# Optimization experiments

Hardware: AMD Instinct MI355X
Metric: run time of the kernel (lower is better)

## Reference

```python
import jax, jax.numpy as jnp
import numpy as np

EMBED = 1024
HIDDEN = 2048
BATCH = 8192


def setup_inputs() -> dict:
    key = jax.random.key(0)
    ks = jax.random.split(key, 14)
    D = EMBED + HIDDEN
    s = 1.0 / np.sqrt(D)
    s2 = 1.0 / np.sqrt(HIDDEN)
    return {
        "x": jax.random.normal(ks[0], (BATCH, EMBED), jnp.float32),
        "short_term": jax.random.normal(ks[1], (BATCH, HIDDEN), jnp.float32),
        "long_term": jax.random.normal(ks[2], (BATCH, HIDDEN), jnp.float32),
        "W_f": jax.random.normal(ks[3], (HIDDEN, D), jnp.float32) * s,
        "b_f": jax.random.normal(ks[4], (HIDDEN,), jnp.float32) * s,
        "W_i": jax.random.normal(ks[5], (HIDDEN, D), jnp.float32) * s,
        "b_i": jax.random.normal(ks[6], (HIDDEN,), jnp.float32) * s,
        "W_c": jax.random.normal(ks[7], (HIDDEN, D), jnp.float32) * s,
        "b_c": jax.random.normal(ks[8], (HIDDEN,), jnp.float32) * s,
        "W_o": jax.random.normal(ks[9], (HIDDEN, D), jnp.float32) * s,
        "b_o": jax.random.normal(ks[10], (HIDDEN,), jnp.float32) * s,
        "W_h2o": jax.random.normal(ks[11], (HIDDEN, HIDDEN), jnp.float32) * s2,
        "b_h2o": jax.random.normal(ks[12], (HIDDEN,), jnp.float32) * s2,
    }


def reference(x, short_term, long_term, W_f, b_f, W_i, b_i, W_c, b_c, W_o, b_o, W_h2o, b_h2o):
    combined = jnp.concatenate([x, short_term], axis=-1)  # [B, E+H]
    # Fuse the four gate linears into one GEMM: [B, E+H] @ [E+H, 4H]
    W_all = jnp.concatenate([W_f, W_i, W_c, W_o], axis=0)  # [4H, E+H]
    b_all = jnp.concatenate([b_f, b_i, b_c, b_o], axis=0)  # [4H]
    gates = combined @ W_all.T + b_all                     # [B, 4H]
    f, i, C, o = jnp.split(gates, 4, axis=-1)
    f = jax.nn.sigmoid(f)
    i = jax.nn.sigmoid(i)
    C = jnp.tanh(C)
    o = jax.nn.sigmoid(o)
    C_new = f * long_term + i * C                          # [B, H]
    C_out = jnp.tanh(C_new @ W_h2o.T + b_h2o)
    output = C_out * o
    return output, C_new
```

## Files before the change

### kernel.cpp

```cpp
#include <hip/hip_runtime.h>
#include <hip/hip_bf16.h>

typedef __bf16 bf16x8 __attribute__((ext_vector_type(8)));
typedef float f32x4 __attribute__((ext_vector_type(4)));

static constexpr int BATCH  = 8192;
static constexpr int EMBED  = 1024;
static constexpr int HIDDEN = 2048;
static constexpr int KD     = EMBED + HIDDEN;

__device__ __forceinline__ float sigm(float x) { return 1.0f / (1.0f + __expf(-x)); }
__device__ __forceinline__ float tanh_fast(float x) { return 2.0f / (1.0f + __expf(-2.0f * x)) - 1.0f; }

__device__ __forceinline__ bf16x8 loadcvt8(const float* __restrict__ p) {
  f32x4 lo = *(const f32x4*)p;
  f32x4 hi = *(const f32x4*)(p + 4);
  bf16x8 r;
  r[0] = (__bf16)lo[0]; r[1] = (__bf16)lo[1]; r[2] = (__bf16)lo[2]; r[3] = (__bf16)lo[3];
  r[4] = (__bf16)hi[0]; r[5] = (__bf16)hi[1]; r[6] = (__bf16)hi[2]; r[7] = (__bf16)hi[3];
  return r;
}

__device__ __forceinline__ void glds16(const void* g, void* l) {
  __builtin_amdgcn_global_load_lds((const __attribute__((address_space(1))) void*)g,
                                   (__attribute__((address_space(3))) void*)l, 16, 0, 0);
}

__global__ __launch_bounds__(256) void cvtA_kernel(const float* __restrict__ x,
                                                   const float* __restrict__ st,
                                                   __bf16* __restrict__ dst) {
  const long i8 = ((long)blockIdx.x * 256 + threadIdx.x) * 8;
  const int r = (int)(i8 / KD);
  const int c = (int)(i8 - (long)r * KD);
  const float* s = (c < EMBED) ? (x + (long)r * EMBED + c)
                               : (st + (long)r * HIDDEN + (c - EMBED));
  *(bf16x8*)(dst + i8) = loadcvt8(s);
}

__global__ __launch_bounds__(256) void cvtW_kernel(const float* __restrict__ Wf,
                                                   const float* __restrict__ Wi,
                                                   const float* __restrict__ Wc,
                                                   const float* __restrict__ Wo,
                                                   __bf16* __restrict__ dst) {
  const int g = blockIdx.y;
  const float* s = (g == 0) ? Wf : (g == 1) ? Wi : (g == 2) ? Wc : Wo;
  const long off = ((long)blockIdx.x * 256 + threadIdx.x) * 8;
  *(bf16x8*)(dst + (long)g * HIDDEN * KD + off) = loadcvt8(s + off);
}

__global__ __launch_bounds__(256) void cvtC_kernel(const float* __restrict__ s,
                                                   __bf16* __restrict__ d) {
  const long off = ((long)blockIdx.x * 256 + threadIdx.x) * 8;
  *(bf16x8*)(d + off) = loadcvt8(s + off);
}

__global__ __launch_bounds__(256, 3) void lstm_gates_kernel(
    const __bf16* __restrict__ A,
    const __bf16* __restrict__ W4,
    const float* __restrict__ lt,
    const float* __restrict__ bfp, const float* __restrict__ bip,
    const float* __restrict__ bcp, const float* __restrict__ bop,
    float* __restrict__ out1, float* __restrict__ out2,
    __bf16* __restrict__ flt, __bf16* __restrict__ ig)
{
  __shared__ __align__(16) __bf16 sA[128 * 32];
  __shared__ __align__(16) __bf16 sB[128 * 32];

  const int tid  = threadIdx.x;
  const int lane = tid & 63;
  const int wave = tid >> 6;
  const int waveM = wave >> 1;
  const int waveN = wave & 1;
  const int gate = blockIdx.z;

  const int row0 = blockIdx.y * 128;
  const int n0   = blockIdx.x * 128;

  const __bf16* __restrict__ Wg = W4 + (long)gate * HIDDEN * KD;

  const int sRow = lane >> 2;
  const int sCol = (lane & 3) * 8;
  const long aA0 = (long)(row0 + wave * 32 +      sRow) * KD + sCol;
  const long aA1 = (long)(row0 + wave * 32 + 16 + sRow) * KD + sCol;
  const long aB0 = (long)(n0   + wave * 32 +      sRow) * KD + sCol;
  const long aB1 = (long)(n0   + wave * 32 + 16 + sRow) * KD + sCol;
  __bf16* lA0 = sA + wave * 1024;
  __bf16* lA1 = sA + wave * 1024 + 512;
  __bf16* lB0 = sB + wave * 1024;
  __bf16* lB1 = sB + wave * 1024 + 512;

  const int kr = (lane >> 4) * 8;
  const int rA = (waveM * 64 + (lane & 15)) * 32 + kr;
  const int rB = (waveN * 64 + (lane & 15)) * 32 + kr;

  f32x4 acc[4][4];
#pragma unroll
  for (int fm = 0; fm < 4; ++fm)
#pragma unroll
    for (int fn = 0; fn < 4; ++fn)
      acc[fm][fn] = (f32x4){0.f, 0.f, 0.f, 0.f};

  for (int k0 = 0; k0 < KD; k0 += 32) {
    __syncthreads();
    glds16(A  + aA0 + k0, lA0);
    glds16(A  + aA1 + k0, lA1);
    glds16(Wg + aB0 + k0, lB0);
    glds16(Wg + aB1 + k0, lB1);
    __syncthreads();

    bf16x8 a[4], b[4];
#pragma unroll
    for (int f = 0; f < 4; ++f) {
      a[f] = *(const bf16x8*)(sA + rA + f * 16 * 32);
      b[f] = *(const bf16x8*)(sB + rB + f * 16 * 32);
    }
#pragma unroll
    for (int fm = 0; fm < 4; ++fm)
#pragma unroll
      for (int fn = 0; fn < 4; ++fn)
        acc[fm][fn] = __builtin_amdgcn_mfma_f32_16x16x32_bf16(a[fm], b[fn], acc[fm][fn], 0, 0, 0);
  }

  const int colB = n0 + waveN * 64 + (lane & 15);
  const int rowB = row0 + waveM * 64 + ((lane >> 4) << 2);

  const float* bias = (gate == 0) ? bfp : (gate == 1) ? bip : (gate == 2) ? bcp : bop;

#pragma unroll
  for (int fn = 0; fn < 4; ++fn) {
    const int col = colB + fn * 16;
    const float bv = bias[col];
#pragma unroll
    for (int fm = 0; fm < 4; ++fm) {
#pragma unroll
      for (int rr = 0; rr < 4; ++rr) {
        const int row = rowB + fm * 16 + rr;
        const size_t idx = (size_t)row * HIDDEN + col;
        const float v = acc[fm][fn][rr] + bv;
        if (gate == 0) {
          flt[idx] = (__bf16)(sigm(v) * lt[idx]);
        } else if (gate == 1) {
          ig[idx] = (__bf16)sigm(v);
        } else if (gate == 2) {
          out2[idx] = tanh_fast(v);
        } else {
          out1[idx] = sigm(v);
        }
      }
    }
  }
}

__global__ __launch_bounds__(256) void lstm_cell_kernel(
    const __bf16* __restrict__ flt, const __bf16* __restrict__ ig,
    float* __restrict__ out2 ,
    __bf16* __restrict__ cnb)
{
  const long i8 = ((long)blockIdx.x * 256 + threadIdx.x) * 8;
  bf16x8 f8 = *(const bf16x8*)(flt + i8);
  bf16x8 i8v = *(const bf16x8*)(ig + i8);
  f32x4 t0 = *(const f32x4*)(out2 + i8);
  f32x4 t1 = *(const f32x4*)(out2 + i8 + 4);
  f32x4 c0, c1;
  bf16x8 cb;
#pragma unroll
  for (int j = 0; j < 4; ++j) {
    c0[j] = (float)f8[j] + (float)i8v[j] * t0[j];
    c1[j] = (float)f8[j + 4] + (float)i8v[j + 4] * t1[j];
    cb[j] = (__bf16)c0[j];
    cb[j + 4] = (__bf16)c1[j];
  }
  *(f32x4*)(out2 + i8) = c0;
  *(f32x4*)(out2 + i8 + 4) = c1;
  *(bf16x8*)(cnb + i8) = cb;
}

__global__ __launch_bounds__(256, 3) void lstm_out_kernel(
    const __bf16* __restrict__ cnb, const __bf16* __restrict__ Whb,
    const float* __restrict__ bh, float* __restrict__ out1)
{
  __shared__ __align__(16) __bf16 sA[128 * 32];
  __shared__ __align__(16) __bf16 sB[128 * 32];

  const int tid  = threadIdx.x;
  const int lane = tid & 63;
  const int wave = tid >> 6;
  const int waveM = wave >> 1;
  const int waveN = wave & 1;

  const int row0 = blockIdx.y * 128;
  const int n0   = blockIdx.x * 128;

  const int sRow = lane >> 2;
  const int sCol = (lane & 3) * 8;
  const long aA0 = (long)(row0 + wave * 32 +      sRow) * HIDDEN + sCol;
  const long aA1 = (long)(row0 + wave * 32 + 16 + sRow) * HIDDEN + sCol;
  const long aB0 = (long)(n0   + wave * 32 +      sRow) * HIDDEN + sCol;
  const long aB1 = (long)(n0   + wave * 32 + 16 + sRow) * HIDDEN + sCol;
  __bf16* lA0 = sA + wave * 1024;
  __bf16* lA1 = sA + wave * 1024 + 512;
  __bf16* lB0 = sB + wave * 1024;
  __bf16* lB1 = sB + wave * 1024 + 512;

  const int kr = (lane >> 4) * 8;
  const int rA = (waveM * 64 + (lane & 15)) * 32 + kr;
  const int rB = (waveN * 64 + (lane & 15)) * 32 + kr;

  f32x4 acc[4][4];
#pragma unroll
  for (int fm = 0; fm < 4; ++fm)
#pragma unroll
    for (int fn = 0; fn < 4; ++fn)
      acc[fm][fn] = (f32x4){0.f, 0.f, 0.f, 0.f};

  for (int k0 = 0; k0 < HIDDEN; k0 += 32) {
    __syncthreads();
    glds16(cnb + aA0 + k0, lA0);
    glds16(cnb + aA1 + k0, lA1);
    glds16(Whb + aB0 + k0, lB0);
    glds16(Whb + aB1 + k0, lB1);
    __syncthreads();

    bf16x8 a[4], b[4];
#pragma unroll
    for (int f = 0; f < 4; ++f) {
      a[f] = *(const bf16x8*)(sA + rA + f * 16 * 32);
      b[f] = *(const bf16x8*)(sB + rB + f * 16 * 32);
    }
#pragma unroll
    for (int fm = 0; fm < 4; ++fm)
#pragma unroll
      for (int fn = 0; fn < 4; ++fn)
        acc[fm][fn] = __builtin_amdgcn_mfma_f32_16x16x32_bf16(a[fm], b[fn], acc[fm][fn], 0, 0, 0);
  }

  const int colB = n0 + waveN * 64 + (lane & 15);
  const int rowB = row0 + waveM * 64 + ((lane >> 4) << 2);
#pragma unroll
  for (int fn = 0; fn < 4; ++fn) {
    const int col = colB + fn * 16;
    const float bv = bh[col];
#pragma unroll
    for (int fm = 0; fm < 4; ++fm) {
#pragma unroll
      for (int rr = 0; rr < 4; ++rr) {
        const int row = rowB + fm * 16 + rr;
        const size_t idx = (size_t)row * HIDDEN + col;
        const float v = tanh_fast(acc[fm][fn][rr] + bv);
        const float ov = out1[idx];
        out1[idx] = v * ov;
      }
    }
  }
}

extern "C" void kernel_launch(void* const* d_in, const int* in_sizes, int n_in,
                              void* d_out, int out_size, void* d_ws, size_t ws_size,
                              hipStream_t stream) {
  const float* x   = (const float*)d_in[0];
  const float* st  = (const float*)d_in[1];
  const float* lt  = (const float*)d_in[2];
  const float* Wf  = (const float*)d_in[3];
  const float* bfp = (const float*)d_in[4];
  const float* Wi  = (const float*)d_in[5];
  const float* bip = (const float*)d_in[6];
  const float* Wc  = (const float*)d_in[7];
  const float* bcp = (const float*)d_in[8];
  const float* Wo  = (const float*)d_in[9];
  const float* bop = (const float*)d_in[10];
  const float* Wh  = (const float*)d_in[11];
  const float* bh  = (const float*)d_in[12];

  float* out1 = (float*)d_out;
  float* out2 = out1 + (size_t)BATCH * HIDDEN;

  __bf16* Ab  = (__bf16*)d_ws;
  __bf16* W4b = Ab + (size_t)BATCH * KD;
  __bf16* Whb = W4b + (size_t)4 * HIDDEN * KD;
  __bf16* Flt = Whb + (size_t)HIDDEN * HIDDEN;
  __bf16* Ig  = Flt + (size_t)BATCH * HIDDEN;
  __bf16* Cnb = Ab;

  cvtA_kernel<<<dim3((BATCH * (long)KD) / 2048), 256, 0, stream>>>(x, st, Ab);
  cvtW_kernel<<<dim3((HIDDEN * (long)KD) / 2048, 4), 256, 0, stream>>>(Wf, Wi, Wc, Wo, W4b);
  cvtC_kernel<<<dim3((HIDDEN * (long)HIDDEN) / 2048), 256, 0, stream>>>(Wh, Whb);

  dim3 grid(HIDDEN / 128, BATCH / 128, 4);
  lstm_gates_kernel<<<grid, 256, 0, stream>>>(Ab, W4b, lt, bfp, bip, bcp, bop,
                                              out1, out2, Flt, Ig);
  lstm_cell_kernel<<<dim3((BATCH * (long)HIDDEN) / 2048), 256, 0, stream>>>(Flt, Ig, out2, Cnb);
  dim3 grid2(HIDDEN / 128, BATCH / 128);
  lstm_out_kernel<<<grid2, 256, 0, stream>>>(Cnb, Whb, bh, out1);
}
```

Before: 1.051 ms.

## Use 256x256 tiles with a 4-stage LDS pipeline, swizzle and block remap for GEMMs

Both GEMM kernels now share a templated 256x256 tile routine run by 512 threads. It uses a 4-deep ring of LDS buffers filled by async global-to-LDS loads, with waitcnt-based fences instead of two syncthreads per K step. LDS addresses are XOR-swizzled to avoid bank conflicts, and block indices are remapped so neighbouring blocks share operands in L2. The 4-gate dimension is folded into the N dimension of a single 2D grid. The intent is higher MFMA utilisation through more data reuse and overlap of loads with compute, at the cost of larger LDS use (128KB), more accumulator registers and lower occupancy.

```diff
diff --git a/kernel.cpp b/kernel.cpp
--- a/kernel.cpp
+++ b/kernel.cpp
@@ -54,7 +54,73 @@
   *(bf16x8*)(d + off) = loadcvt8(s + off);
 }
 
-__global__ __launch_bounds__(256, 3) void lstm_gates_kernel(
+template<int LDA, int LDB, int NT>
+__device__ __forceinline__ void gemm256(const __bf16* __restrict__ Agl,
+                                        const __bf16* __restrict__ Bgl,
+                                        f32x4 (&acc)[8][4])
+{
+  __shared__ __align__(16) __bf16 lds[4][2][256 * 32];
+
+  const int tid  = threadIdx.x;
+  const int lane = tid & 63;
+  const int w    = tid >> 6;
+
+  const int sRow = lane >> 2;
+  const int sCol = (((lane & 3) ^ (lane >> 4)) << 3);
+  const __bf16* gA = Agl + (size_t)(w * 16 + sRow) * LDA + sCol;
+  const __bf16* gB = Bgl + (size_t)(w * 16 + sRow) * LDB + sCol;
+  const int ldsLo = w * 512;
+  const int ldsHi = (w + 8) * 512;
+
+  const int rm    = lane & 15;
+  const int rdCol = (((lane >> 4) ^ ((lane >> 2) & 3)) << 3);
+  const int aOff  = ((w >> 2) * 128 + rm) * 32 + rdCol;
+  const int bOff  = ((w & 3) * 64 + rm) * 32 + rdCol;
+
+  auto stage = [&](int b, int jt) {
+    const size_t ko = (size_t)jt * 32;
+    glds16(gA + ko,                     &lds[b][0][ldsLo]);
+    glds16(gA + ko + (size_t)128 * LDA, &lds[b][0][ldsHi]);
+    glds16(gB + ko,                     &lds[b][1][ldsLo]);
+    glds16(gB + ko + (size_t)128 * LDB, &lds[b][1][ldsHi]);
+  };
+
+  auto fence = [&]() {
+    __builtin_amdgcn_sched_barrier(0);
+    asm volatile("s_waitcnt vmcnt(8)" ::: "memory");
+    __builtin_amdgcn_sched_barrier(0);
+    __builtin_amdgcn_s_barrier();
+    __builtin_amdgcn_sched_barrier(0);
+  };
+
+  stage(0, 0); stage(1, 1); stage(2, 2);
+  fence();
+
+  auto step = [&](int b, int jt) {
+    if (jt + 3 < NT) stage((b + 3) & 3, jt + 3);
+    bf16x8 aF[8], bF[4];
+#pragma unroll
+    for (int fm = 0; fm < 8; ++fm)
+      aF[fm] = *(const bf16x8*)&lds[b][0][aOff + fm * 512];
+#pragma unroll
+    for (int fn = 0; fn < 4; ++fn)
+      bF[fn] = *(const bf16x8*)&lds[b][1][bOff + fn * 512];
+    __builtin_amdgcn_s_setprio(1);
+#pragma unroll
+    for (int fm = 0; fm < 8; ++fm)
+#pragma unroll
+      for (int fn = 0; fn < 4; ++fn)
+        acc[fm][fn] = __builtin_amdgcn_mfma_f32_16x16x32_bf16(aF[fm], bF[fn], acc[fm][fn], 0, 0, 0);
+    __builtin_amdgcn_s_setprio(0);
+    fence();
+  };
+
+  for (int jt = 0; jt < NT; jt += 4) {
+    step(0, jt); step(1, jt + 1); step(2, jt + 2); step(3, jt + 3);
+  }
+}
+
+__global__ __launch_bounds__(512, 2) void lstm_gates_kernel(
     const __bf16* __restrict__ A,
     const __bf16* __restrict__ W4,
     const float* __restrict__ lt,
@@ -63,67 +129,29 @@
     float* __restrict__ out1, float* __restrict__ out2,
     __bf16* __restrict__ flt, __bf16* __restrict__ ig)
 {
-  __shared__ __align__(16) __bf16 sA[128 * 32];
-  __shared__ __align__(16) __bf16 sB[128 * 32];
+  int lin = blockIdx.y * 32 + blockIdx.x;
+  lin = (lin & 7) * 128 + (lin >> 3);
+  const int bx = lin & 31;
+  const int by = lin >> 5;
+
+  const int row0 = by * 256;
+  const int n0f  = bx * 256;
+
+  f32x4 acc[8][4];
+#pragma unroll
+  for (int fm = 0; fm < 8; ++fm)
+#pragma unroll
+    for (int fn = 0; fn < 4; ++fn)
+      acc[fm][fn] = (f32x4){0.f, 0.f, 0.f, 0.f};
+
+  gemm256<KD, KD, KD / 32>(A + (size_t)row0 * KD, W4 + (size_t)n0f * KD, acc);
 
   const int tid  = threadIdx.x;
   const int lane = tid & 63;
-  const int wave = tid >> 6;
-  const int waveM = wave >> 1;
-  const int waveN = wave & 1;
-  const int gate = blockIdx.z;
-
-  const int row0 = blockIdx.y * 128;
-  const int n0   = blockIdx.x * 128;
-
-  const __bf16* __restrict__ Wg = W4 + (long)gate * HIDDEN * KD;
-
-  const int sRow = lane >> 2;
-  const int sCol = (lane & 3) * 8;
-  const long aA0 = (long)(row0 + wave * 32 +      sRow) * KD + sCol;
-  const long aA1 = (long)(row0 + wave * 32 + 16 + sRow) * KD + sCol;
-  const long aB0 = (long)(n0   + wave * 32 +      sRow) * KD + sCol;
-  const long aB1 = (long)(n0   + wave * 32 + 16 + sRow) * KD + sCol;
-  __bf16* lA0 = sA + wave * 1024;
-  __bf16* lA1 = sA + wave * 1024 + 512;
-  __bf16* lB0 = sB + wave * 1024;
-  __bf16* lB1 = sB + wave * 1024 + 512;
-
-  const int kr = (lane >> 4) * 8;
-  const int rA = (waveM * 64 + (lane & 15)) * 32 + kr;
-  const int rB = (waveN * 64 + (lane & 15)) * 32 + kr;
-
-  f32x4 acc[4][4];
-#pragma unroll
-  for (int fm = 0; fm < 4; ++fm)
-#pragma unroll
-    for (int fn = 0; fn < 4; ++fn)
-      acc[fm][fn] = (f32x4){0.f, 0.f, 0.f, 0.f};
-
-  for (int k0 = 0; k0 < KD; k0 += 32) {
-    __syncthreads();
-    glds16(A  + aA0 + k0, lA0);
-    glds16(A  + aA1 + k0, lA1);
-    glds16(Wg + aB0 + k0, lB0);
-    glds16(Wg + aB1 + k0, lB1);
-    __syncthreads();
-
-    bf16x8 a[4], b[4];
-#pragma unroll
-    for (int f = 0; f < 4; ++f) {
-      a[f] = *(const bf16x8*)(sA + rA + f * 16 * 32);
-      b[f] = *(const bf16x8*)(sB + rB + f * 16 * 32);
-    }
-#pragma unroll
-    for (int fm = 0; fm < 4; ++fm)
-#pragma unroll
-      for (int fn = 0; fn < 4; ++fn)
-        acc[fm][fn] = __builtin_amdgcn_mfma_f32_16x16x32_bf16(a[fm], b[fn], acc[fm][fn], 0, 0, 0);
-  }
-
-  const int colB = n0 + waveN * 64 + (lane & 15);
-  const int rowB = row0 + waveM * 64 + ((lane >> 4) << 2);
-
+  const int w    = tid >> 6;
+  const int gate = n0f >> 11;
+  const int colB = (n0f & 2047) + (w & 3) * 64 + (lane & 15);
+  const int rowB = row0 + (w >> 2) * 128 + ((lane >> 4) << 2);
   const float* bias = (gate == 0) ? bfp : (gate == 1) ? bip : (gate == 2) ? bcp : bop;
 
 #pragma unroll
@@ -131,7 +159,7 @@
     const int col = colB + fn * 16;
     const float bv = bias[col];
 #pragma unroll
-    for (int fm = 0; fm < 4; ++fm) {
+    for (int fm = 0; fm < 8; ++fm) {
 #pragma unroll
       for (int rr = 0; rr < 4; ++rr) {
         const int row = rowB + fm * 16 + rr;
@@ -175,73 +203,40 @@
   *(bf16x8*)(cnb + i8) = cb;
 }
 
-__global__ __launch_bounds__(256, 3) void lstm_out_kernel(
+__global__ __launch_bounds__(512, 2) void lstm_out_kernel(
     const __bf16* __restrict__ cnb, const __bf16* __restrict__ Whb,
     const float* __restrict__ bh, float* __restrict__ out1)
 {
-  __shared__ __align__(16) __bf16 sA[128 * 32];
-  __shared__ __align__(16) __bf16 sB[128 * 32];
+  int lin = blockIdx.y * 8 + blockIdx.x;
+  lin = (lin & 7) * 32 + (lin >> 3);
+  const int bx = lin & 7;
+  const int by = lin >> 3;
+
+  const int row0 = by * 256;
+  const int n0   = bx * 256;
+
+  f32x4 acc[8][4];
+#pragma unroll
+  for (int fm = 0; fm < 8; ++fm)
+#pragma unroll
+    for (int fn = 0; fn < 4; ++fn)
+      acc[fm][fn] = (f32x4){0.f, 0.f, 0.f, 0.f};
+
+  gemm256<HIDDEN, HIDDEN, HIDDEN / 32>(cnb + (size_t)row0 * HIDDEN,
+                                       Whb + (size_t)n0 * HIDDEN, acc);
 
   const int tid  = threadIdx.x;
   const int lane = tid & 63;
-  const int wave = tid >> 6;
-  const int waveM = wave >> 1;
-  const int waveN = wave & 1;
-
-  const int row0 = blockIdx.y * 128;
-  const int n0   = blockIdx.x * 128;
-
-  const int sRow = lane >> 2;
-  const int sCol = (lane & 3) * 8;
-  const long aA0 = (long)(row0 + wave * 32 +      sRow) * HIDDEN + sCol;
-  const long aA1 = (long)(row0 + wave * 32 + 16 + sRow) * HIDDEN + sCol;
-  const long aB0 = (long)(n0   + wave * 32 +      sRow) * HIDDEN + sCol;
-  const long aB1 = (long)(n0   + wave * 32 + 16 + sRow) * HIDDEN + sCol;
-  __bf16* lA0 = sA + wave * 1024;
-  __bf16* lA1 = sA + wave * 1024 + 512;
-  __bf16* lB0 = sB + wave * 1024;
-  __bf16* lB1 = sB + wave * 1024 + 512;
-
-  const int kr = (lane >> 4) * 8;
-  const int rA = (waveM * 64 + (lane & 15)) * 32 + kr;
-  const int rB = (waveN * 64 + (lane & 15)) * 32 + kr;
-
-  f32x4 acc[4][4];
-#pragma unroll
-  for (int fm = 0; fm < 4; ++fm)
-#pragma unroll
-    for (int fn = 0; fn < 4; ++fn)
-      acc[fm][fn] = (f32x4){0.f, 0.f, 0.f, 0.f};
-
-  for (int k0 = 0; k0 < HIDDEN; k0 += 32) {
-    __syncthreads();
-    glds16(cnb + aA0 + k0, lA0);
-    glds16(cnb + aA1 + k0, lA1);
-    glds16(Whb + aB0 + k0, lB0);
-    glds16(Whb + aB1 + k0, lB1);
-    __syncthreads();
-
-    bf16x8 a[4], b[4];
-#pragma unroll
-    for (int f = 0; f < 4; ++f) {
-      a[f] = *(const bf16x8*)(sA + rA + f * 16 * 32);
-      b[f] = *(const bf16x8*)(sB + rB + f * 16 * 32);
-    }
-#pragma unroll
-    for (int fm = 0; fm < 4; ++fm)
-#pragma unroll
-      for (int fn = 0; fn < 4; ++fn)
-        acc[fm][fn] = __builtin_amdgcn_mfma_f32_16x16x32_bf16(a[fm], b[fn], acc[fm][fn], 0, 0, 0);
-  }
-
-  const int colB = n0 + waveN * 64 + (lane & 15);
-  const int rowB = row0 + waveM * 64 + ((lane >> 4) << 2);
+  const int w    = tid >> 6;
+  const int colB = n0 + (w & 3) * 64 + (lane & 15);
+  const int rowB = row0 + (w >> 2) * 128 + ((lane >> 4) << 2);
+
 #pragma unroll
   for (int fn = 0; fn < 4; ++fn) {
     const int col = colB + fn * 16;
     const float bv = bh[col];
 #pragma unroll
-    for (int fm = 0; fm < 4; ++fm) {
+    for (int fm = 0; fm < 8; ++fm) {
 #pragma unroll
       for (int rr = 0; rr < 4; ++rr) {
         const int row = rowB + fm * 16 + rr;
@@ -285,10 +280,10 @@
   cvtW_kernel<<<dim3((HIDDEN * (long)KD) / 2048, 4), 256, 0, stream>>>(Wf, Wi, Wc, Wo, W4b);
   cvtC_kernel<<<dim3((HIDDEN * (long)HIDDEN) / 2048), 256, 0, stream>>>(Wh, Whb);
 
-  dim3 grid(HIDDEN / 128, BATCH / 128, 4);
-  lstm_gates_kernel<<<grid, 256, 0, stream>>>(Ab, W4b, lt, bfp, bip, bcp, bop,
-                                              out1, out2, Flt, Ig);
+  dim3 grid1(8192 / 256, BATCH / 256);
+  lstm_gates_kernel<<<grid1, 512, 0, stream>>>(Ab, W4b, lt, bfp, bip, bcp, bop,
+                                               out1, out2, Flt, Ig);
   lstm_cell_kernel<<<dim3((BATCH * (long)HIDDEN) / 2048), 256, 0, stream>>>(Flt, Ig, out2, Cnb);
-  dim3 grid2(HIDDEN / 128, BATCH / 128);
-  lstm_out_kernel<<<grid2, 256, 0, stream>>>(Cnb, Whb, bh, out1);
-}
+  dim3 grid2(HIDDEN / 256, BATCH / 256);
+  lstm_out_kernel<<<grid2, 512, 0, stream>>>(Cnb, Whb, bh, out1);
+}
```

New measurement: 955.0 us. 9.1% less time.
